# Optimization experiments

Hardware: AMD Instinct MI355X
Metric: run time of the kernel (lower is better)

## Reference

```python
import jax, jax.numpy as jnp
import numpy as np

EPS = 1e-5  # BatchNorm eps (torch default)


def setup_inputs() -> dict:
    key = jax.random.key(0)
    ks = jax.random.split(key, 12)
    B, T, F = 2048, 128, 84

    def rn(k, sh, scale=0.05):
        return jax.random.normal(k, sh, jnp.float32) * scale

    return {
        "x": jax.random.normal(ks[0], (B, T, F), jnp.float32),
        # Conv1d(84 -> 64, k=3, pad=1)
        "conv1d_w": rn(ks[1], (64, F, 3)),
        "conv1d_b": rn(ks[2], (64,)),
        # BatchNorm1d(64), eval mode (running stats)
        "bn_gamma": jnp.ones((64,), jnp.float32),
        "bn_beta": jnp.zeros((64,), jnp.float32),
        "bn_mean": jnp.zeros((64,), jnp.float32),
        "bn_var": jnp.ones((64,), jnp.float32),
        # Linear(64*16 -> 64*4*4)
        "lin_w": rn(ks[3], (1024, 1024)),
        "lin_b": rn(ks[4], (1024,)),
        # ConvLSTM cell: Conv2d(192 -> 512, k=3, pad=1, groups=4)
        "cell_w": rn(ks[5], (512, 48, 3, 3)),
        "cell_b": rn(ks[6], (512,)),
        # Classifier
        "cls1_w": rn(ks[7], (128, 2048)),
        "cls1_b": rn(ks[8], (128,)),
        "cls2_w": rn(ks[9], (2, 128)),
        "cls2_b": rn(ks[10], (2,)),
    }


def reference(x, conv1d_w, conv1d_b, bn_gamma, bn_beta, bn_mean, bn_var,
              lin_w, lin_b, cell_w, cell_b, cls1_w, cls1_b, cls2_w, cls2_b):
    B, T, F = x.shape
    H = 128  # hidden channels

    # Per-timestep encoder is state-free -> vectorize over (B, T).
    # Conv1d k=3 pad=1 on a length-1 sequence: only the center tap hits data.
    enc = jnp.einsum('btf,cf->btc', x, conv1d_w[:, :, 1]) + conv1d_b  # [B,T,64]
    enc = (enc - bn_mean) * (bn_gamma / jnp.sqrt(bn_var + EPS)) + bn_beta
    enc = jax.nn.relu(enc)
    # flatten of [64,16] is channel-major -> repeat along last axis.
    flat = jnp.repeat(enc, 16, axis=-1)                               # [B,T,1024]
    to2d = jnp.einsum('btk,ok->bto', flat, lin_w) + lin_b             # [B,T,1024]
    xt = to2d.reshape(B, T, 64, 4, 4).transpose(1, 0, 2, 3, 4)        # [T,B,64,4,4]

    def step(carry, x_t):
        h, c = carry
        comb = jnp.concatenate([x_t, h], axis=1)                      # [B,192,4,4]
        conv = jax.lax.conv_general_dilated(
            comb, cell_w, window_strides=(1, 1), padding='SAME',
            dimension_numbers=('NCHW', 'OIHW', 'NCHW'),
            feature_group_count=4)
        conv = conv + cell_b[None, :, None, None]                     # [B,512,4,4]
        cc_i, cc_f, cc_o, cc_g = jnp.split(conv, 4, axis=1)
        c_next = jax.nn.sigmoid(cc_f) * c + jax.nn.sigmoid(cc_i) * jnp.tanh(cc_g)
        h_next = jax.nn.sigmoid(cc_o) * jnp.tanh(c_next)
        return (h_next, c_next), None

    h0 = jnp.zeros((B, H, 4, 4), x.dtype)
    (h_last, _), _ = jax.lax.scan(step, (h0, h0), xt)

    feat = h_last.reshape(B, H * 16)                                  # [B,2048]
    hid = jax.nn.relu(feat @ cls1_w.T + cls1_b)
    return hid @ cls2_w.T + cls2_b                                    # [B,2]
```

## Files before the change

kernel.cpp:

```cpp
#include <hip/hip_runtime.h>
#include <math.h>

#define BN_EPS 1e-5f

typedef _Float16 f16x8 __attribute__((ext_vector_type(8)));
typedef _Float16 f16x2 __attribute__((ext_vector_type(2)));
typedef unsigned short u16x8 __attribute__((ext_vector_type(8)));
typedef float f32x4 __attribute__((ext_vector_type(4)));
typedef float f32x16 __attribute__((ext_vector_type(16)));


__global__ void prep_enc_w(const float* __restrict__ conv1d_w,
                           const float* __restrict__ conv1d_b,
                           const float* __restrict__ gamma,
                           const float* __restrict__ beta,
                           const float* __restrict__ mean,
                           const float* __restrict__ var,
                           float* __restrict__ We, float* __restrict__ be) {
  int tid = blockIdx.x * blockDim.x + threadIdx.x;
  if (tid < 5376) {
    int c = tid / 84, f = tid % 84;
    float s = gamma[c] * rsqrtf(var[c] + BN_EPS);
    We[c * 84 + f] = s * conv1d_w[c * 252 + f * 3 + 1];
    if (f == 0) be[c] = s * conv1d_b[c] + (beta[c] - mean[c] * s);
  }
}

__global__ void prep_wef(const float* __restrict__ We, _Float16* __restrict__ WeF) {
  int tid = blockIdx.x * blockDim.x + threadIdx.x;
  if (tid >= 6144) return;
  int j = tid & 7, lane = (tid >> 3) & 63, kch = (tid >> 9) % 3, ct = tid / 1536;
  int c = ct * 16 + (lane & 15);
  int k = kch * 32 + (lane >> 4) * 8 + j;
  WeF[tid] = (k < 84) ? (_Float16)We[c * 84 + k] : (_Float16)0.f;
}

__global__ void prep_w2(const float* __restrict__ lin_w, float* __restrict__ W2) {
  int tid = blockIdx.x * blockDim.x + threadIdx.x;
  int o2 = tid >> 6, c = tid & 63;
  float s = 0.f;
#pragma unroll
  for (int j = 0; j < 16; ++j) s += lin_w[o2 * 1024 + c * 16 + j];
  W2[o2 * 64 + c] = s;
}

__global__ void prep_A(const float* __restrict__ cell_w,
                       const float* __restrict__ cell_b,
                       const float* __restrict__ lin_b,
                       const float* __restrict__ W2,
                       float* __restrict__ A, float* __restrict__ Abias) {
  int tid = blockIdx.x * blockDim.x + threadIdx.x;
  int go = tid >> 10;
  int c = (tid >> 4) & 63;
  int p = tid & 15;
  int y = p >> 2, x = p & 3;
  int kn = (go >= 128) ? 16 : 48;
  int xb = (go >= 128) ? 48 : 0;
  float a = 0.f;
  for (int k = 0; k < kn; ++k)
    for (int dy = 0; dy < 3; ++dy) {
      int yy = y + dy - 1;
      if (yy < 0 || yy > 3) continue;
      for (int dx = 0; dx < 3; ++dx) {
        int xx = x + dx - 1;
        if (xx < 0 || xx > 3) continue;
        a += cell_w[((go * 48 + k) * 3 + dy) * 3 + dx] *
             W2[((xb + k) * 16 + yy * 4 + xx) * 64 + c];
      }
    }
  A[(go * 64 + c) * 16 + p] = a;
  if (c == 0) {
    float bs = cell_b[go];
    for (int k = 0; k < kn; ++k)
      for (int dy = 0; dy < 3; ++dy) {
        int yy = y + dy - 1;
        if (yy < 0 || yy > 3) continue;
        for (int dx = 0; dx < 3; ++dx) {
          int xx = x + dx - 1;
          if (xx < 0 || xx > 3) continue;
          bs += cell_w[((go * 48 + k) * 3 + dy) * 3 + dx] *
                lin_b[(xb + k) * 16 + yy * 4 + xx];
        }
      }
    Abias[go * 16 + p] = bs;
  }
}

__global__ void pack_a16(const float* __restrict__ A, _Float16* __restrict__ Apk) {
  int tid = blockIdx.x * blockDim.x + threadIdx.x;
  int j = tid & 7, lane = (tid >> 3) & 63, kch = (tid >> 9) & 1, go = tid >> 10;
  int p = lane & 15;
  int c = kch * 32 + (lane >> 4) * 8 + j;
  Apk[tid] = (_Float16)A[(go * 64 + c) * 16 + p];
}

__global__ void pack_wcv(const float* __restrict__ cell_w, _Float16* __restrict__ Wcv) {
  int tid = blockIdx.x * blockDim.x + threadIdx.x;
  int j = tid & 7, lane = (tid >> 3) & 63, m = (tid >> 9) & 3, tmk = tid >> 11;
  int co = m * 32 + (lane & 31);
  int khi = (lane >> 5) * 8 + j;
  float v;
  if (tmk < 18) {
    int kch = tmk / 9, tap = tmk % 9;
    v = cell_w[((size_t)(128 + co) * 48 + 16 + kch * 16 + khi) * 9 + tap];
  } else if (tmk < 45) {
    int r = tmk - 18; int kch = r / 9, tap = r % 9;
    v = cell_w[((size_t)(256 + co) * 48 + kch * 16 + khi) * 9 + tap];
  } else {
    int r = tmk - 45; int kch = r / 9, tap = r % 9;
    v = cell_w[((size_t)(384 + co) * 48 + kch * 16 + khi) * 9 + tap];
  }
  Wcv[tid] = (_Float16)v;
}

__device__ __forceinline__ float sigm(float v) {
  return __fdividef(1.f, 1.f + __expf(-v));
}
__device__ __forceinline__ float tanh_fast(float v) {
  return 1.f - __fdividef(2.f, __expf(2.f * v) + 1.f);
}

__global__ __launch_bounds__(256, 3) void xgate_kernel(
    const float* __restrict__ x, const _Float16* __restrict__ WeF,
    const float* __restrict__ be, const _Float16* __restrict__ Apk,
    const float* __restrict__ Abias, unsigned short* __restrict__ sixf, int tc) {
  __shared__ __align__(16) _Float16 x16[128 * 104];
  __shared__ __align__(16) _Float16 enc_s[128 * 72];
  int tid = threadIdx.x, lane = tid & 63, w = tid >> 6;
  int gq = blockIdx.x >> 7, cq = blockIdx.x & 127;
  int n = lane & 15, kgrp = lane >> 4;

  const float* xb = x + ((size_t)cq * 16 * 128 + (size_t)tc * 8) * 84;
  for (int i = tid; i < 10752; i += 256) {
    int ccl = i / 84, kk = i - ccl * 84;
    int bloc = ccl >> 3, trel = ccl & 7;
    x16[ccl * 104 + kk] = (_Float16)xb[(size_t)bloc * 10752 + trel * 84 + kk];
  }
  for (int i = tid; i < 2560; i += 256) {
    int ccl = i / 20, kk = 84 + (i - ccl * 20);
    x16[ccl * 104 + kk] = (_Float16)0.f;
  }
  __syncthreads();

  for (int ct4 = 0; ct4 < 8; ++ct4) {
    f32x4 acc = *(const f32x4*)(be + w * 16 + kgrp * 4);
#pragma unroll
    for (int kch = 0; kch < 3; ++kch)
      acc = __builtin_amdgcn_mfma_f32_16x16x32_f16(
          *(const f16x8*)(WeF + ((w * 3 + kch) * 64 + lane) * 8),
          *(const f16x8*)(&x16[(ct4 * 16 + n) * 104 + kch * 32 + kgrp * 8]),
          acc, 0, 0, 0);
#pragma unroll
    for (int r = 0; r < 4; ++r)
      enc_s[(ct4 * 16 + n) * 72 + w * 16 + kgrp * 4 + r] =
          (_Float16)fmaxf(acc[r], 0.f);
  }
  __syncthreads();

  for (int ct4 = 0; ct4 < 8; ++ct4) {
    int ccl = ct4 * 16 + n;
    int b = cq * 16 + (ccl >> 3), trel = ccl & 7;
#pragma unroll 2
    for (int gol = 0; gol < 16; ++gol) {
      int go = gq * 64 + w * 16 + gol;
      f32x4 acc = *(const f32x4*)(Abias + go * 16 + kgrp * 4);
      acc = __builtin_amdgcn_mfma_f32_16x16x32_f16(
          *(const f16x8*)(Apk + (size_t)go * 1024 + lane * 8),
          *(const f16x8*)(&enc_s[ccl * 72 + kgrp * 8]), acc, 0, 0, 0);
      acc = __builtin_amdgcn_mfma_f32_16x16x32_f16(
          *(const f16x8*)(Apk + (size_t)go * 1024 + 512 + lane * 8),
          *(const f16x8*)(&enc_s[ccl * 72 + 32 + kgrp * 8]), acc, 0, 0, 0);
      int ch = go & 127, slot = go >> 7;
      unsigned short* dst =
          sixf + ((((size_t)b * 8 + trel) * 128 + ch) * 2 + slot) * 16 + kgrp * 4;
      if (slot == 0) {
#pragma unroll
        for (int rp = 0; rp < 2; ++rp) {
          unsigned lo = (unsigned)(sigm(acc[rp * 2]) * 65535.f + 0.5f);
          unsigned hi = (unsigned)(sigm(acc[rp * 2 + 1]) * 65535.f + 0.5f);
          *(unsigned*)(dst + rp * 2) = lo | (hi << 16);
        }
      } else {
#pragma unroll
        for (int rp = 0; rp < 2; ++rp) {
          f16x2 pv = {(_Float16)acc[rp * 2], (_Float16)acc[rp * 2 + 1]};
          *(f16x2*)(dst + rp * 2) = pv;
        }
      }
    }
  }
}

#define HPB 4624
#define HPQ 272
#define ZQ 4352
#define COFF 36992
#define GOFF 102528
#define GSZ 18432
#define LDSZ 157824

__device__ __forceinline__ void cell_update(
    unsigned char* lds, const unsigned short* __restrict__ sixf_b,
    _Float16* __restrict__ h16_b, int ch, int bl, int hf, int t,
    float cbo, float cbg, bool lastT) {
  int b = hf * 4 + bl;
  int cell = hf * 512 + ch * 4 + bl;
  const unsigned short* sp = sixf_b + (((size_t)b * 8 + t) * 128 + ch) * 32;
  const _Float16* Gf = (const _Float16*)(lds + GOFF + 0 * GSZ + ch * 144 + bl * 32);
  const _Float16* Go = (const _Float16*)(lds + GOFF + 1 * GSZ + ch * 144 + bl * 32);
  const _Float16* Gg = (const _Float16*)(lds + GOFF + 2 * GSZ + ch * 144 + bl * 32);
  float* cp = (float*)(lds + COFF) + cell;
#pragma unroll
  for (int h8 = 0; h8 < 2; ++h8) {
    u16x8 s = *(const u16x8*)(sp + h8 * 8);
    f16x8 xv = *(const f16x8*)(sp + 16 + h8 * 8);
    f16x8 gfv = *(const f16x8*)(Gf + h8 * 8);
    f16x8 gov = *(const f16x8*)(Go + h8 * 8);
    f16x8 ggv = *(const f16x8*)(Gg + h8 * 8);
#pragma unroll
    for (int j = 0; j < 8; ++j) {
      int p = h8 * 8 + j;
      float si = (float)s[j] * (1.f / 65535.f);
      float xf = (float)xv[j];
      float cold = cp[p * 1024];
      float cv = sigm(xf + (float)gfv[j]) * cold +
                 si * tanh_fast(cbg + (float)ggv[j]);
      cp[p * 1024] = cv;
      float hn = sigm(cbo + (float)gov[j]) * tanh_fast(cv);
      *(_Float16*)(lds + b * HPB + p * HPQ + ch * 2) = (_Float16)hn;
      if (lastT) h16_b[((size_t)b * 16 + p) * 128 + ch] = (_Float16)hn;
    }
  }
}

template <int GATE>
__device__ __forceinline__ void role_loop(
    unsigned char* lds, const _Float16* __restrict__ Wg,
    const unsigned short* __restrict__ sixf_b,
    _Float16* __restrict__ h16_b, const float* __restrict__ cell_b,
    int m, int lane, int tid, const unsigned* tapbase, unsigned gwbase) {
  constexpr int NKCH = (GATE == 0) ? 2 : 3;
  constexpr unsigned CIOFF = (GATE == 0) ? 0u : (GATE == 1 ? 64u : 160u);
  f16x8 wr[NKCH * 9];
#pragma unroll
  for (int fi = 0; fi < NKCH * 9; ++fi)
    wr[fi] = *(const f16x8*)(Wg + (size_t)(fi * 4 + m) * 512 + (lane << 3));

  int idx = (GATE == 2) ? (tid - 256) : tid;
  int ch = idx >> 2, bl = idx & 3;
  constexpr bool own0 = (GATE != 2), own1 = (GATE != 1);
  float cbo = cell_b[256 + ch], cbg = cell_b[384 + ch];

  for (int t = 0; t < 8; ++t) {
#pragma unroll
    for (int hf = 0; hf < 2; ++hf) {
#pragma unroll
      for (int nt = 0; nt < 2; ++nt) {
        unsigned bofs = (unsigned)(hf * 4 + nt * 2) * HPB;
        f32x16 acc = {};
#pragma unroll
        for (int kch = 0; kch < NKCH; ++kch)
#pragma unroll
          for (int tap = 0; tap < 9; ++tap)
            acc = __builtin_amdgcn_mfma_f32_32x32x16_f16(
                wr[kch * 9 + tap],
                *(const f16x8*)(lds + tapbase[tap] + bofs + CIOFF +
                                (unsigned)kch * 32),
                acc, 0, 0, 0);
#pragma unroll
        for (int r = 0; r < 16; ++r) {
          unsigned co_l = (unsigned)((r & 3) + 8 * (r >> 2));
          *(_Float16*)(lds + gwbase + (unsigned)GATE * GSZ + co_l * 144u +
                       (unsigned)nt * 64u) = (_Float16)acc[r];
        }
      }
      __syncthreads();
      if (hf == 0) {
        if (own0) cell_update(lds, sixf_b, h16_b, ch, bl, 0, t, cbo, cbg, t == 7);
      } else {
        if (own1) cell_update(lds, sixf_b, h16_b, ch, bl, 1, t, cbo, cbg, t == 7);
      }
      __syncthreads();
    }
  }
}

__global__ __launch_bounds__(768, 3) void recur8_kernel(
    const unsigned short* __restrict__ sixf, const _Float16* __restrict__ Wcv,
    const float* __restrict__ cell_b, _Float16* __restrict__ h16,
    float* __restrict__ cstate) {
  __shared__ __align__(16) unsigned char lds[LDSZ];
  int tid = threadIdx.x, lane = tid & 63, w = tid >> 6;
  int gate = w >> 2, m = w & 3;

  _Float16* h16_b = h16 + (size_t)blockIdx.x * 16384;
  for (int i = tid; i < 16384; i += 768) {
    int bl8 = i >> 11, q = (i >> 7) & 15, chh = i & 127;
    *(_Float16*)(lds + bl8 * HPB + q * HPQ + chh * 2) = h16_b[i];
  }
  for (int i = tid; i < 1024; i += 768) {
    int bl8 = i >> 7, chh = i & 127;
    *(_Float16*)(lds + bl8 * HPB + ZQ + chh * 2) = (_Float16)0.f;
  }
  float* cl = (float*)(lds + COFF);
  float* cst_b = cstate + (size_t)blockIdx.x * 16384;
  for (int i = tid; i < 16384; i += 768) cl[i] = cst_b[i];

  int col = lane & 31, khalf = lane >> 5, b_lo = col >> 4, p_c = col & 15;
  int yc = p_c >> 2, xc = p_c & 3;
  unsigned tapbase[9];
#pragma unroll
  for (int dy = 0; dy < 3; ++dy)
#pragma unroll
    for (int dx = 0; dx < 3; ++dx) {
      int qy = yc + dy - 1, qx = xc + dx - 1;
      bool valid = (qy >= 0 && qy < 4 && qx >= 0 && qx < 4);
      tapbase[dy * 3 + dx] =
          (valid ? (unsigned)((qy * 4 + qx) * HPQ) : (unsigned)ZQ) +
          (unsigned)(b_lo * HPB + khalf * 16);
    }
  unsigned gwbase = (unsigned)GOFF + (unsigned)((m * 32 + khalf * 4) * 144) +
                    (unsigned)(b_lo * 32 + p_c * 2);
  __syncthreads();

  const unsigned short* sixf_b = sixf + (size_t)blockIdx.x * 262144;
  if (gate == 0)
    role_loop<0>(lds, Wcv, sixf_b, h16_b, cell_b, m, lane, tid, tapbase, gwbase);
  else if (gate == 1)
    role_loop<1>(lds, Wcv + 36864, sixf_b, h16_b, cell_b, m, lane, tid, tapbase, gwbase);
  else
    role_loop<2>(lds, Wcv + 92160, sixf_b, h16_b, cell_b, m, lane, tid, tapbase, gwbase);

  for (int i = tid; i < 16384; i += 768) cst_b[i] = cl[i];
}

__global__ __launch_bounds__(128) void cls_kernel(
    const _Float16* __restrict__ h16, const float* __restrict__ w1,
    const float* __restrict__ b1, const float* __restrict__ w2,
    const float* __restrict__ b2, float* __restrict__ out) {
  __shared__ __align__(16) float feat[8 * 2064];
  __shared__ float hid[8 * 128];
  int b0 = blockIdx.x * 8;
  for (int i = threadIdx.x; i < 16384; i += 128) {
    int bl = i >> 11, r = i & 2047, p = r >> 7, chh = r & 127;
    feat[bl * 2064 + chh * 16 + p] = (float)h16[(size_t)b0 * 2048 + i];
  }
  __syncthreads();
  int ch = threadIdx.x;
  float acc[8];
#pragma unroll
  for (int b = 0; b < 8; ++b) acc[b] = b1[ch];
  const float4* wr = (const float4*)(w1 + (size_t)ch * 2048);
  for (int k4 = 0; k4 < 512; ++k4) {
    float4 wv = wr[k4];
#pragma unroll
    for (int b = 0; b < 8; ++b) {
      float4 f = *(const float4*)(&feat[b * 2064 + k4 * 4]);
      acc[b] += wv.x * f.x + wv.y * f.y + wv.z * f.z + wv.w * f.w;
    }
  }
#pragma unroll
  for (int b = 0; b < 8; ++b) hid[b * 128 + ch] = fmaxf(acc[b], 0.f);
  __syncthreads();
  if (threadIdx.x < 16) {
    int b = threadIdx.x >> 1, o = threadIdx.x & 1;
    float s = b2[o];
    for (int k = 0; k < 128; ++k) s += hid[b * 128 + k] * w2[o * 128 + k];
    out[(size_t)(b0 + b) * 2 + o] = s;
  }
}

extern "C" void kernel_launch(void* const* d_in, const int* in_sizes, int n_in,
                              void* d_out, int out_size, void* d_ws, size_t ws_size,
                              hipStream_t stream) {
  const float* x        = (const float*)d_in[0];
  const float* conv1d_w = (const float*)d_in[1];
  const float* conv1d_b = (const float*)d_in[2];
  const float* bn_gamma = (const float*)d_in[3];
  const float* bn_beta  = (const float*)d_in[4];
  const float* bn_mean  = (const float*)d_in[5];
  const float* bn_var   = (const float*)d_in[6];
  const float* lin_w    = (const float*)d_in[7];
  const float* lin_b    = (const float*)d_in[8];
  const float* cell_w   = (const float*)d_in[9];
  const float* cell_b   = (const float*)d_in[10];
  const float* cls1_w   = (const float*)d_in[11];
  const float* cls1_b   = (const float*)d_in[12];
  const float* cls2_w   = (const float*)d_in[13];
  const float* cls2_b   = (const float*)d_in[14];

  float* ws = (float*)d_ws;
  float* We    = ws + 0;
  float* be    = ws + 8192;
  float* W2    = ws + 12288;
  float* A     = ws + 81920;
  float* Abias = ws + 344064;
  _Float16* WeF = (_Float16*)(ws + 348160);
  _Float16* Apk = (_Float16*)(ws + 352256);
  _Float16* Wcv = (_Float16*)(ws + 483328);
  _Float16* h16 = (_Float16*)(ws + 557056);
  float* cstate = ws + 2654208;
  unsigned short* sixf = (unsigned short*)(ws + 6848512);
  float* out = (float*)d_out;

  prep_enc_w<<<21, 256, 0, stream>>>(conv1d_w, conv1d_b, bn_gamma, bn_beta,
                                     bn_mean, bn_var, We, be);
  prep_wef<<<24, 256, 0, stream>>>(We, WeF);
  prep_w2<<<256, 256, 0, stream>>>(lin_w, W2);
  prep_A<<<1024, 256, 0, stream>>>(cell_w, cell_b, lin_b, W2, A, Abias);
  pack_a16<<<1024, 256, 0, stream>>>(A, Apk);
  pack_wcv<<<576, 256, 0, stream>>>(cell_w, Wcv);
  hipMemsetAsync(h16, 0, 8388608, stream);
  hipMemsetAsync(cstate, 0, 16777216, stream);
  for (int tc = 0; tc < 16; ++tc) {
    xgate_kernel<<<512, 256, 0, stream>>>(x, WeF, be, Apk, Abias, sixf, tc);
    recur8_kernel<<<256, 768, 0, stream>>>(sixf, Wcv, cell_b, h16, cstate);
  }
  cls_kernel<<<256, 128, 0, stream>>>(h16, cls1_w, cls1_b, cls2_w, cls2_b, out);
}
```

Before: 3.871 ms.

## Apply gate activations in MFMA epilogue and prefetch per-step inputs before MMA

Moves the sigmoid/tanh for the output and candidate gates, plus their bias add, into the MFMA writeback of the gate-1 and gate-2 waves. The biases are staged in LDS for this. Cell-update threads then read already-activated values, which shortens the serial section between barriers. The per-step precomputed input slices are loaded from global memory before the MFMA loop so their latency overlaps compute. In exchange, activations are stored in fp16, which costs precision, and extra registers are held across the MMA loop, which may affect occupancy.

```diff
diff --git a/kernel.cpp b/kernel.cpp
--- a/kernel.cpp
+++ b/kernel.cpp
@@ -197,23 +197,22 @@
 #define COFF 36992
 #define GOFF 102528
 #define GSZ 18432
-#define LDSZ 157824
+#define CBOFF 157824
+#define LDSZ 158848
 
 __device__ __forceinline__ void cell_update(
-    unsigned char* lds, const unsigned short* __restrict__ sixf_b,
-    _Float16* __restrict__ h16_b, int ch, int bl, int hf, int t,
-    float cbo, float cbg, bool lastT) {
+    unsigned char* lds, u16x8 s0, u16x8 s1, f16x8 x0, f16x8 x1,
+    _Float16* __restrict__ h16_b, int ch, int bl, int hf, bool lastT) {
   int b = hf * 4 + bl;
   int cell = hf * 512 + ch * 4 + bl;
-  const unsigned short* sp = sixf_b + (((size_t)b * 8 + t) * 128 + ch) * 32;
   const _Float16* Gf = (const _Float16*)(lds + GOFF + 0 * GSZ + ch * 144 + bl * 32);
   const _Float16* Go = (const _Float16*)(lds + GOFF + 1 * GSZ + ch * 144 + bl * 32);
   const _Float16* Gg = (const _Float16*)(lds + GOFF + 2 * GSZ + ch * 144 + bl * 32);
   float* cp = (float*)(lds + COFF) + cell;
 #pragma unroll
   for (int h8 = 0; h8 < 2; ++h8) {
-    u16x8 s = *(const u16x8*)(sp + h8 * 8);
-    f16x8 xv = *(const f16x8*)(sp + 16 + h8 * 8);
+    u16x8 s = h8 ? s1 : s0;
+    f16x8 xv = h8 ? x1 : x0;
     f16x8 gfv = *(const f16x8*)(Gf + h8 * 8);
     f16x8 gov = *(const f16x8*)(Go + h8 * 8);
     f16x8 ggv = *(const f16x8*)(Gg + h8 * 8);
@@ -221,12 +220,11 @@
     for (int j = 0; j < 8; ++j) {
       int p = h8 * 8 + j;
       float si = (float)s[j] * (1.f / 65535.f);
-      float xf = (float)xv[j];
+      float fg = sigm((float)xv[j] + (float)gfv[j]);
       float cold = cp[p * 1024];
-      float cv = sigm(xf + (float)gfv[j]) * cold +
-                 si * tanh_fast(cbg + (float)ggv[j]);
+      float cv = fg * cold + si * (float)ggv[j];
       cp[p * 1024] = cv;
-      float hn = sigm(cbo + (float)gov[j]) * tanh_fast(cv);
+      float hn = (float)gov[j] * tanh_fast(cv);
       *(_Float16*)(lds + b * HPB + p * HPQ + ch * 2) = (_Float16)hn;
       if (lastT) h16_b[((size_t)b * 16 + p) * 128 + ch] = (_Float16)hn;
     }
@@ -237,7 +235,7 @@
 __device__ __forceinline__ void role_loop(
     unsigned char* lds, const _Float16* __restrict__ Wg,
     const unsigned short* __restrict__ sixf_b,
-    _Float16* __restrict__ h16_b, const float* __restrict__ cell_b,
+    _Float16* __restrict__ h16_b,
     int m, int lane, int tid, const unsigned* tapbase, unsigned gwbase) {
   constexpr int NKCH = (GATE == 0) ? 2 : 3;
   constexpr unsigned CIOFF = (GATE == 0) ? 0u : (GATE == 1 ? 64u : 160u);
@@ -249,11 +247,22 @@
   int idx = (GATE == 2) ? (tid - 256) : tid;
   int ch = idx >> 2, bl = idx & 3;
   constexpr bool own0 = (GATE != 2), own1 = (GATE != 1);
-  float cbo = cell_b[256 + ch], cbg = cell_b[384 + ch];
+  int cobase = m * 32 + (lane >> 5) * 4;
 
   for (int t = 0; t < 8; ++t) {
 #pragma unroll
     for (int hf = 0; hf < 2; ++hf) {
+      bool me = hf == 0 ? own0 : own1;
+      u16x8 s0, s1;
+      f16x8 x0, x1;
+      if (me) {
+        const unsigned short* sp =
+            sixf_b + (((size_t)(hf * 4 + bl) * 8 + t) * 128 + ch) * 32;
+        s0 = *(const u16x8*)(sp);
+        s1 = *(const u16x8*)(sp + 8);
+        x0 = *(const f16x8*)(sp + 16);
+        x1 = *(const f16x8*)(sp + 24);
+      }
 #pragma unroll
       for (int nt = 0; nt < 2; ++nt) {
         unsigned bofs = (unsigned)(hf * 4 + nt * 2) * HPB;
@@ -270,16 +279,17 @@
 #pragma unroll
         for (int r = 0; r < 16; ++r) {
           unsigned co_l = (unsigned)((r & 3) + 8 * (r >> 2));
+          float v = acc[r];
+          if (GATE == 1)
+            v = sigm(*(const float*)(lds + CBOFF + (unsigned)(cobase + (int)co_l) * 4u) + v);
+          else if (GATE == 2)
+            v = tanh_fast(*(const float*)(lds + CBOFF + 512u + (unsigned)(cobase + (int)co_l) * 4u) + v);
           *(_Float16*)(lds + gwbase + (unsigned)GATE * GSZ + co_l * 144u +
-                       (unsigned)nt * 64u) = (_Float16)acc[r];
+                       (unsigned)nt * 64u) = (_Float16)v;
         }
       }
       __syncthreads();
-      if (hf == 0) {
-        if (own0) cell_update(lds, sixf_b, h16_b, ch, bl, 0, t, cbo, cbg, t == 7);
-      } else {
-        if (own1) cell_update(lds, sixf_b, h16_b, ch, bl, 1, t, cbo, cbg, t == 7);
-      }
+      if (me) cell_update(lds, s0, s1, x0, x1, h16_b, ch, bl, hf, t == 7);
       __syncthreads();
     }
   }
@@ -305,6 +315,7 @@
   float* cl = (float*)(lds + COFF);
   float* cst_b = cstate + (size_t)blockIdx.x * 16384;
   for (int i = tid; i < 16384; i += 768) cl[i] = cst_b[i];
+  if (tid < 256) *(float*)(lds + CBOFF + tid * 4) = cell_b[256 + tid];
 
   int col = lane & 31, khalf = lane >> 5, b_lo = col >> 4, p_c = col & 15;
   int yc = p_c >> 2, xc = p_c & 3;
@@ -325,11 +336,11 @@
 
   const unsigned short* sixf_b = sixf + (size_t)blockIdx.x * 262144;
   if (gate == 0)
-    role_loop<0>(lds, Wcv, sixf_b, h16_b, cell_b, m, lane, tid, tapbase, gwbase);
+    role_loop<0>(lds, Wcv, sixf_b, h16_b, m, lane, tid, tapbase, gwbase);
   else if (gate == 1)
-    role_loop<1>(lds, Wcv + 36864, sixf_b, h16_b, cell_b, m, lane, tid, tapbase, gwbase);
+    role_loop<1>(lds, Wcv + 36864, sixf_b, h16_b, m, lane, tid, tapbase, gwbase);
   else
-    role_loop<2>(lds, Wcv + 92160, sixf_b, h16_b, cell_b, m, lane, tid, tapbase, gwbase);
+    role_loop<2>(lds, Wcv + 92160, sixf_b, h16_b, m, lane, tid, tapbase, gwbase);
 
   for (int i = tid; i < 16384; i += 768) cst_b[i] = cl[i];
 }
```

After: 5.038 ms. 30.1% more time.

## Stage xgate outputs through LDS for coalesced stores and split sixf layout

Applied to the files above, without the earlier changes.

Changes the sixf intermediate layout from interleaved [ch][slot][16] to slot-major [slot][ch][16] per (b,t). xgate_kernel now stages each wave's MFMA outputs in an LDS tile and writes them back as contiguous 16-byte vector stores, instead of scattering 8-byte stores. The x load is vectorised to float4 per row. The goal is to cut uncoalesced global traffic in the x-gate producer and to hoist the consumer's loads in cell_update. The cost is extra LDS, explicit waitcnt/sched barriers, and a layout both kernels must agree on.

```diff
diff --git a/kernel.cpp b/kernel.cpp
--- a/kernel.cpp
+++ b/kernel.cpp
@@ -4,6 +4,7 @@
 #define BN_EPS 1e-5f
 
 typedef _Float16 f16x8 __attribute__((ext_vector_type(8)));
+typedef _Float16 f16x4 __attribute__((ext_vector_type(4)));
 typedef _Float16 f16x2 __attribute__((ext_vector_type(2)));
 typedef unsigned short u16x8 __attribute__((ext_vector_type(8)));
 typedef float f32x4 __attribute__((ext_vector_type(4)));
@@ -126,19 +127,30 @@
     const float* __restrict__ Abias, unsigned short* __restrict__ sixf, int tc) {
   __shared__ __align__(16) _Float16 x16[128 * 104];
   __shared__ __align__(16) _Float16 enc_s[128 * 72];
+  __shared__ __align__(16) unsigned char Tt[4 * 2304];
   int tid = threadIdx.x, lane = tid & 63, w = tid >> 6;
   int gq = blockIdx.x >> 7, cq = blockIdx.x & 127;
   int n = lane & 15, kgrp = lane >> 4;
 
-  const float* xb = x + ((size_t)cq * 16 * 128 + (size_t)tc * 8) * 84;
-  for (int i = tid; i < 10752; i += 256) {
-    int ccl = i / 84, kk = i - ccl * 84;
-    int bloc = ccl >> 3, trel = ccl & 7;
-    x16[ccl * 104 + kk] = (_Float16)xb[(size_t)bloc * 10752 + trel * 84 + kk];
-  }
-  for (int i = tid; i < 2560; i += 256) {
-    int ccl = i / 20, kk = 84 + (i - ccl * 20);
-    x16[ccl * 104 + kk] = (_Float16)0.f;
+  {
+    int r = tid >> 1, half = tid & 1;
+    int b = cq * 16 + (r >> 3), t = tc * 8 + (r & 7);
+    const float* rowp = x + ((size_t)b * 128 + t) * 84;
+#pragma unroll
+    for (int j = 0; j < 11; ++j) {
+      int q = half + 2 * j;
+      if (q < 21) {
+        float4 v = *(const float4*)(rowp + q * 4);
+        f16x4 h;
+        h[0] = (_Float16)v.x; h[1] = (_Float16)v.y;
+        h[2] = (_Float16)v.z; h[3] = (_Float16)v.w;
+        *(f16x4*)(&x16[r * 104 + q * 4]) = h;
+      }
+    }
+    for (int i = tid; i < 4096; i += 256) {
+      int rr = i >> 5, k = i & 31;
+      if (k < 20) x16[rr * 104 + 84 + k] = (_Float16)0.f;
+    }
   }
   __syncthreads();
 
@@ -157,36 +169,53 @@
   }
   __syncthreads();
 
+  int slotB = gq >> 1;
+  int chbase = (gq & 1) * 64 + w * 16;
+  unsigned char* Tw = Tt + w * 2304;
+  int fn = lane >> 2;
   for (int ct4 = 0; ct4 < 8; ++ct4) {
     int ccl = ct4 * 16 + n;
-    int b = cq * 16 + (ccl >> 3), trel = ccl & 7;
-#pragma unroll 2
-    for (int gol = 0; gol < 16; ++gol) {
-      int go = gq * 64 + w * 16 + gol;
-      f32x4 acc = *(const f32x4*)(Abias + go * 16 + kgrp * 4);
-      acc = __builtin_amdgcn_mfma_f32_16x16x32_f16(
-          *(const f16x8*)(Apk + (size_t)go * 1024 + lane * 8),
-          *(const f16x8*)(&enc_s[ccl * 72 + kgrp * 8]), acc, 0, 0, 0);
-      acc = __builtin_amdgcn_mfma_f32_16x16x32_f16(
-          *(const f16x8*)(Apk + (size_t)go * 1024 + 512 + lane * 8),
-          *(const f16x8*)(&enc_s[ccl * 72 + 32 + kgrp * 8]), acc, 0, 0, 0);
-      int ch = go & 127, slot = go >> 7;
-      unsigned short* dst =
-          sixf + ((((size_t)b * 8 + trel) * 128 + ch) * 2 + slot) * 16 + kgrp * 4;
-      if (slot == 0) {
-#pragma unroll
-        for (int rp = 0; rp < 2; ++rp) {
-          unsigned lo = (unsigned)(sigm(acc[rp * 2]) * 65535.f + 0.5f);
-          unsigned hi = (unsigned)(sigm(acc[rp * 2 + 1]) * 65535.f + 0.5f);
-          *(unsigned*)(dst + rp * 2) = lo | (hi << 16);
+    int fb = cq * 16 + ct4 * 2 + (fn >> 3), ftr = fn & 7;
+    size_t grow =
+        (((size_t)fb * 8 + ftr) * 2 + slotB) * 2048 + (size_t)chbase * 16;
+    for (int gb = 0; gb < 4; ++gb) {
+#pragma unroll
+      for (int gi = 0; gi < 4; ++gi) {
+        int gol = gb * 4 + gi;
+        int go = gq * 64 + w * 16 + gol;
+        f32x4 acc = *(const f32x4*)(Abias + go * 16 + kgrp * 4);
+        acc = __builtin_amdgcn_mfma_f32_16x16x32_f16(
+            *(const f16x8*)(Apk + (size_t)go * 1024 + lane * 8),
+            *(const f16x8*)(&enc_s[ccl * 72 + kgrp * 8]), acc, 0, 0, 0);
+        acc = __builtin_amdgcn_mfma_f32_16x16x32_f16(
+            *(const f16x8*)(Apk + (size_t)go * 1024 + 512 + lane * 8),
+            *(const f16x8*)(&enc_s[ccl * 72 + 32 + kgrp * 8]), acc, 0, 0, 0);
+        unsigned char* tdst = Tw + n * 144 + gi * 32 + kgrp * 8;
+        if (gq < 2) {
+#pragma unroll
+          for (int rp = 0; rp < 2; ++rp) {
+            unsigned lo = (unsigned)(sigm(acc[rp * 2]) * 65535.f + 0.5f);
+            unsigned hi = (unsigned)(sigm(acc[rp * 2 + 1]) * 65535.f + 0.5f);
+            *(unsigned*)(tdst + rp * 4) = lo | (hi << 16);
+          }
+        } else {
+#pragma unroll
+          for (int rp = 0; rp < 2; ++rp) {
+            f16x2 pv = {(_Float16)acc[rp * 2], (_Float16)acc[rp * 2 + 1]};
+            *(f16x2*)(tdst + rp * 4) = pv;
+          }
         }
-      } else {
-#pragma unroll
-        for (int rp = 0; rp < 2; ++rp) {
-          f16x2 pv = {(_Float16)acc[rp * 2], (_Float16)acc[rp * 2 + 1]};
-          *(f16x2*)(dst + rp * 2) = pv;
-        }
-      }
+      }
+      asm volatile("s_waitcnt lgkmcnt(0)" ::: "memory");
+      __builtin_amdgcn_sched_barrier(0);
+#pragma unroll
+      for (int j = 0; j < 2; ++j) {
+        int chunk = (lane & 3) + 4 * j;
+        f16x8 v = *(const f16x8*)(Tw + fn * 144 + chunk * 16);
+        *(f16x8*)(sixf + grow + (size_t)gb * 64 + (size_t)chunk * 8) = v;
+      }
+      asm volatile("s_waitcnt lgkmcnt(0)" ::: "memory");
+      __builtin_amdgcn_sched_barrier(0);
     }
   }
 }
@@ -205,15 +234,19 @@
     float cbo, float cbg, bool lastT) {
   int b = hf * 4 + bl;
   int cell = hf * 512 + ch * 4 + bl;
-  const unsigned short* sp = sixf_b + (((size_t)b * 8 + t) * 128 + ch) * 32;
+  const unsigned short* sp = sixf_b + ((size_t)b * 8 + t) * 4096 + ch * 16;
+  u16x8 s0 = *(const u16x8*)(sp);
+  u16x8 s1 = *(const u16x8*)(sp + 8);
+  f16x8 x0 = *(const f16x8*)(sp + 2048);
+  f16x8 x1 = *(const f16x8*)(sp + 2056);
   const _Float16* Gf = (const _Float16*)(lds + GOFF + 0 * GSZ + ch * 144 + bl * 32);
   const _Float16* Go = (const _Float16*)(lds + GOFF + 1 * GSZ + ch * 144 + bl * 32);
   const _Float16* Gg = (const _Float16*)(lds + GOFF + 2 * GSZ + ch * 144 + bl * 32);
   float* cp = (float*)(lds + COFF) + cell;
 #pragma unroll
   for (int h8 = 0; h8 < 2; ++h8) {
-    u16x8 s = *(const u16x8*)(sp + h8 * 8);
-    f16x8 xv = *(const f16x8*)(sp + 16 + h8 * 8);
+    u16x8 s = h8 ? s1 : s0;
+    f16x8 xv = h8 ? x1 : x0;
     f16x8 gfv = *(const f16x8*)(Gf + h8 * 8);
     f16x8 gov = *(const f16x8*)(Go + h8 * 8);
     f16x8 ggv = *(const f16x8*)(Gg + h8 * 8);
```

Result: faster. 3.513 ms (median of 2 runs) (-9.3%).
